# Performance work log

Hardware: AMD Instinct MI355X
Metric: run time of the kernel (lower is better)

The kernel has to match this reference:

```python
import jax, jax.numpy as jnp
import numpy as np

B, S, D, H = 4, 2048, 1024, 16
HS = D // H  # head size = 64


def setup_inputs() -> dict:
    key = jax.random.key(0)
    k1, k2, k3 = jax.random.split(key, 3)
    return {
        "input_data": jax.random.normal(k1, (B, S, D), dtype=jnp.float32),
        "w_qkv": jax.random.normal(k2, (D, 3 * D), dtype=jnp.float32) * (1.0 / np.sqrt(D)),
        "b_qkv": jnp.zeros((3 * D,), dtype=jnp.float32),
        "w_proj": jax.random.normal(k3, (D, D), dtype=jnp.float32) * (1.0 / np.sqrt(D)),
        "b_proj": jnp.zeros((D,), dtype=jnp.float32),
    }


def reference(input_data, w_qkv, b_qkv, w_proj, b_proj):
    b, s, d = input_data.shape
    qkv = input_data @ w_qkv + b_qkv  # [b, s, 3d]
    q, k, v = jnp.split(qkv, 3, axis=-1)
    # [b, h, s, hs]
    q = q.reshape(b, s, H, HS).transpose(0, 2, 1, 3)
    k = k.reshape(b, s, H, HS).transpose(0, 2, 1, 3)
    v = v.reshape(b, s, H, HS).transpose(0, 2, 1, 3)
    # NB: original module scales by 1/sqrt(num_heads), not 1/sqrt(head_size)
    scores = jnp.einsum('bhqd,bhkd->bhqk', q, k) / jnp.sqrt(jnp.float32(H))
    causal = jnp.tril(jnp.ones((s, s), dtype=bool))
    scores = jnp.where(causal[None, None], scores, -jnp.inf)
    weights = jax.nn.softmax(scores, axis=-1)  # dropout p=0.0 -> identity
    out = jnp.einsum('bhqk,bhkd->bhqd', weights, v)
    out = out.transpose(0, 2, 1, 3).reshape(b, s, d)
    return out @ w_proj + b_proj
```

## Files before the change

kernel.cpp:

```cpp
#include <hip/hip_runtime.h>


typedef unsigned short u16;
typedef short bf16x8 __attribute__((ext_vector_type(8)));
typedef unsigned short u16x8 __attribute__((ext_vector_type(8)));
typedef float f32x4 __attribute__((ext_vector_type(4)));
typedef float f32x16 __attribute__((ext_vector_type(16)));

#define S_LEN 2048
#define DMODEL 1024
#define NHEAD 16
#define MROWS 8192

#define SCALE_LOG2E 0.36067376022224085f
#define DEFER_THR 8.0f

__device__ __forceinline__ u16 f2bf(float f) {
  union { float f; unsigned u; } c; c.f = f;
  unsigned u = c.u;
  u += 0x7fffu + ((u >> 16) & 1u);
  return (u16)(u >> 16);
}

__device__ __forceinline__ float exp2_fast(float x) {
  float r; asm("v_exp_f32 %0, %1" : "=v"(r) : "v"(x)); return r;
}

__device__ __forceinline__ unsigned cvtpk_bf16(float a, float b) {
  unsigned r;
  asm("v_cvt_pk_bf16_f32 %0, %1, %2" : "=v"(r) : "v"(a), "v"(b));
  return r;
}

__device__ __forceinline__ void plswap(unsigned& a, unsigned& b) {
  asm("v_permlane32_swap_b32 %0, %1" : "+v"(a), "+v"(b));
}

__device__ __forceinline__ f32x4 mfma16(bf16x8 a, bf16x8 b, f32x4 c) {
  return __builtin_amdgcn_mfma_f32_16x16x32_bf16(a, b, c, 0, 0, 0);
}

__device__ __forceinline__ f32x16 mfma32(bf16x8 a, bf16x8 b, f32x16 c) {
  return __builtin_amdgcn_mfma_f32_32x32x16_bf16(a, b, c, 0, 0, 0);
}

__device__ __forceinline__ void gload_lds16(const void* g, void* l) {
  __builtin_amdgcn_global_load_lds((__attribute__((address_space(1))) void*)g,
                                   (__attribute__((address_space(3))) void*)l,
                                   16, 0, 0);
}

__global__ void k_f32_to_bf16(const float* __restrict__ in, u16* __restrict__ out, int n) {
  int i = (blockIdx.x * 256 + threadIdx.x) * 4;
  if (i < n) {
    float4 v = *reinterpret_cast<const float4*>(in + i);
    ushort4 o;
    o.x = f2bf(v.x); o.y = f2bf(v.y); o.z = f2bf(v.z); o.w = f2bf(v.w);
    *reinterpret_cast<ushort4*>(out + i) = o;
  }
}

__global__ void k_transpose_to_bf16(const float* __restrict__ in, u16* __restrict__ out,
                                    int K, int N) {
  __shared__ float t[32][33];
  int n0 = blockIdx.x * 32, k0 = blockIdx.y * 32;
  int tx = threadIdx.x & 31, ty = threadIdx.x >> 5;
#pragma unroll
  for (int i = 0; i < 32; i += 8)
    t[ty + i][tx] = in[(size_t)(k0 + ty + i) * N + n0 + tx];
  __syncthreads();
#pragma unroll
  for (int i = 0; i < 32; i += 8)
    out[(size_t)(n0 + ty + i) * K + k0 + tx] = f2bf(t[tx][ty + i]);
}

template <int MODE>
__global__ __launch_bounds__(512, 1) void k_gemm8(const u16* __restrict__ A,
                                                  const u16* __restrict__ Bt,
                                                  const float* __restrict__ bias,
                                                  u16* __restrict__ outb,
                                                  float* __restrict__ outf,
                                                  u16* __restrict__ vtout,
                                                  int N, int K) {
  __shared__ u16 As[2][2][256 * 32];
  __shared__ u16 Bs[2][2][128 * 32];

  const int tid = threadIdx.x;
  const int lane = tid & 63, wave = tid >> 6;
  const int wr = wave >> 1, wc = wave & 1;
  const int lr = lane & 15, lk = lane >> 4;
  const int m0 = blockIdx.x * 256, n0 = blockIdx.y * 128;
  const size_t Kb = (size_t)K * 2;

  const int csw = ((tid & 3) ^ ((tid >> 3) & 3)) * 16;
  const char* Asrc0 = (const char*)A + (size_t)(m0 + (tid >> 2)) * Kb + csw;
  const char* Asrc1 = Asrc0 + 128 * Kb;
  const char* Bsrc0 = (const char*)Bt + (size_t)(n0 + (tid >> 2)) * Kb + csw;

#define STAGE_KH(BUFX, KH, T)                                                  \
  {                                                                            \
    const size_t ko_ = (size_t)(T) * 128 + (KH) * 64;                          \
    gload_lds16(Asrc0 + ko_, &As[BUFX][KH][(size_t)tid * 8]);                  \
    gload_lds16(Asrc1 + ko_, &As[BUFX][KH][((size_t)tid + 512) * 8]);          \
    gload_lds16(Bsrc0 + ko_, &Bs[BUFX][KH][(size_t)tid * 8]);                  \
  }

  f32x4 zero4 = {0.f, 0.f, 0.f, 0.f};
  f32x4 acc[4][4];
#pragma unroll
  for (int m = 0; m < 4; ++m)
#pragma unroll
    for (int n = 0; n < 4; ++n) acc[m][n] = zero4;

  const int slotsw = (lr >> 1) & 3;

#define PHASE(BUFX, KH, T, DOSTAGE, VMZERO)                                    \
  {                                                                            \
    if (VMZERO) asm volatile("s_waitcnt vmcnt(0)" ::: "memory");               \
    else        asm volatile("s_waitcnt vmcnt(3)" ::: "memory");               \
    __builtin_amdgcn_s_barrier();                                              \
    __builtin_amdgcn_sched_barrier(0);                                         \
    bf16x8 af[4], bfr[4];                                                      \
    _Pragma("unroll") for (int m = 0; m < 4; ++m)                              \
        af[m] = *reinterpret_cast<const bf16x8*>(                              \
            &As[BUFX][KH][(wr * 64 + m * 16 + lr) * 32 + ((lk ^ slotsw) * 8)]);\
    _Pragma("unroll") for (int n = 0; n < 4; ++n)                              \
        bfr[n] = *reinterpret_cast<const bf16x8*>(                             \
            &Bs[BUFX][KH][(wc * 64 + n * 16 + lr) * 32 + ((lk ^ slotsw) * 8)]);\
    if (DOSTAGE) STAGE_KH((BUFX) ^ 1, KH, (T) + 1);                            \
    __builtin_amdgcn_sched_barrier(0);                                         \
    __builtin_amdgcn_s_setprio(1);                                             \
    _Pragma("unroll") for (int m = 0; m < 4; ++m)                              \
        _Pragma("unroll") for (int n = 0; n < 4; ++n)                          \
            acc[m][n] = mfma16(af[m], bfr[n], acc[m][n]);                      \
    __builtin_amdgcn_s_setprio(0);                                             \
  }

  const int nkt = K >> 6;
  STAGE_KH(0, 0, 0);
  STAGE_KH(0, 1, 0);

  for (int t = 0; t < nkt - 1; ++t) {
    const int buf = t & 1;
    PHASE(buf, 0, t, 1, 0);
    PHASE(buf, 1, t, 1, 0);
  }
  {
    const int buf = (nkt - 1) & 1;
    PHASE(buf, 0, nkt - 1, 0, 0);
    PHASE(buf, 1, nkt - 1, 0, 1);
  }
#undef PHASE
#undef STAGE_KH

#pragma unroll
  for (int n = 0; n < 4; ++n) {
    int col = n0 + wc * 64 + n * 16 + lr;
    float bv = bias[col];
#pragma unroll
    for (int m = 0; m < 4; ++m) {
      int rowb = m0 + wr * 64 + m * 16 + lk * 4;
      if (MODE == 1) {
#pragma unroll
        for (int r = 0; r < 4; ++r)
          outf[(size_t)(rowb + r) * N + col] = acc[m][n][r] + bv;
      } else {
        if (col < 2048) {
          const float qs = (col < 1024) ? SCALE_LOG2E : 1.0f;
#pragma unroll
          for (int r = 0; r < 4; ++r)
            outb[(size_t)(rowb + r) * 2048 + col] = f2bf((acc[m][n][r] + bv) * qs);
        } else {
          int hh = (col >> 6) & 15, dd = col & 63;
          int bb = rowb >> 11, ss = rowb & 2047;
          ushort4 o;
          o.x = f2bf(acc[m][n][0] + bv);
          o.y = f2bf(acc[m][n][1] + bv);
          o.z = f2bf(acc[m][n][2] + bv);
          o.w = f2bf(acc[m][n][3] + bv);
          *reinterpret_cast<ushort4*>(
              vtout + ((size_t)(bb * 16 + hh) * 64 + dd) * 2048 + ss) = o;
        }
      }
    }
  }
}

__global__ __launch_bounds__(512, 4) void k_attn7(const u16* __restrict__ qk,
                                                  const u16* __restrict__ vt,
                                                  u16* __restrict__ ao) {
  __shared__ u16 Ks[2][4096];
  __shared__ u16 Vs[2][4096];

  const int tid = threadIdx.x;
  const int lane = tid & 63, wave = tid >> 6;
  const int l31 = lane & 31, hi = lane >> 5;
  const int gid = blockIdx.x;
  const int bh = gid & 63;
  const int tq = gid >> 6;
  const int t = (tq < 4) ? tq : 11 - tq;
  const int b = bh >> 4, h = bh & 15;

  const int q0 = t * 256 + wave * 32;
  const int ktd = (q0 + 31) >> 6;
  const int KTMAX = 4 * t + 3;
  const int qrel = q0 + l31 - ktd * 64;

  bf16x8 qf[4];
  {
    const u16* qp = qk + ((size_t)b * S_LEN + q0 + l31) * 2048 + h * 64 + hi * 8;
#pragma unroll
    for (int ks = 0; ks < 4; ++ks)
      qf[ks] = *reinterpret_cast<const bf16x8*>(qp + ks * 16);
  }

  const int swzcol = 16 * ((lane & 7) ^ (lane >> 3));
  const char* kg = (const char*)qk + ((size_t)b * S_LEN) * 4096 + 2048 + h * 128 +
                   (size_t)(wave * 8 + (lane >> 3)) * 4096 + swzcol;
  const char* vg = (const char*)vt +
                   ((size_t)bh * 64 + wave * 8 + (lane >> 3)) * 4096 + swzcol;

#define STAGE(BUF, KT)                                                   \
  {                                                                      \
    gload_lds16(kg + (size_t)(KT) * 64 * 4096, &Ks[BUF][wave * 512]);    \
    gload_lds16(vg + (size_t)(KT) * 128, &Vs[BUF][wave * 512]);          \
  }

  f32x16 oT[2];
#pragma unroll
  for (int kb = 0; kb < 2; ++kb)
#pragma unroll
    for (int g = 0; g < 16; ++g) oT[kb][g] = 0.f;
  float m_i = -INFINITY;
  float l_i = 0.f;

  const int rsw = (l31 & 7) << 4;

  STAGE(0, 0);
  __syncthreads();
  int buf = 0;

  for (int kt = 0; kt <= KTMAX; ++kt) {
    if (kt < KTMAX) STAGE(buf ^ 1, kt + 1);

    if (kt <= ktd) {
      const char* Kb = (const char*)&Ks[buf][0];
      const char* Vb = (const char*)&Vs[buf][0];
      const bool masked = (kt == ktd);

      bf16x8 kf[2][4];
#pragma unroll
      for (int kb = 0; kb < 2; ++kb)
#pragma unroll
        for (int ks = 0; ks < 4; ++ks)
          kf[kb][ks] = *reinterpret_cast<const bf16x8*>(
              Kb + (kb * 32 + l31) * 128 + ((ks * 32 + hi * 16) ^ rsw));

      f32x16 sc[2];
#pragma unroll
      for (int kb = 0; kb < 2; ++kb) {
        sc[kb] = mfma32(kf[kb][0], qf[0], f32x16{});
#pragma unroll
        for (int ks = 1; ks < 4; ++ks) sc[kb] = mfma32(kf[kb][ks], qf[ks], sc[kb]);
      }

      bf16x8 vf[2][4];
#pragma unroll
      for (int kbd = 0; kbd < 2; ++kbd)
#pragma unroll
        for (int tt = 0; tt < 4; ++tt)
          vf[kbd][tt] = *reinterpret_cast<const bf16x8*>(
              Vb + (kbd * 32 + l31) * 128 + ((tt * 32 + hi * 16) ^ rsw));

      if (masked) {
#pragma unroll
        for (int kb = 0; kb < 2; ++kb)
#pragma unroll
          for (int g = 0; g < 16; ++g) {
            int key_ = kb * 32 + (g & 3) + ((g >> 2) << 3) + hi * 4;
            if (key_ > qrel) sc[kb][g] = -INFINITY;
          }
      }
      float mxa = fmaxf(sc[0][0], sc[0][4]), mxb = fmaxf(sc[0][1], sc[0][5]);
      float mxc = fmaxf(sc[0][2], sc[0][6]), mxd = fmaxf(sc[0][3], sc[0][7]);
#pragma unroll
      for (int g = 8; g < 16; g += 4) {
        mxa = fmaxf(mxa, sc[0][g]);     mxb = fmaxf(mxb, sc[0][g + 1]);
        mxc = fmaxf(mxc, sc[0][g + 2]); mxd = fmaxf(mxd, sc[0][g + 3]);
      }
#pragma unroll
      for (int g = 0; g < 16; g += 4) {
        mxa = fmaxf(mxa, sc[1][g]);     mxb = fmaxf(mxb, sc[1][g + 1]);
        mxc = fmaxf(mxc, sc[1][g + 2]); mxd = fmaxf(mxd, sc[1][g + 3]);
      }
      float mx = fmaxf(fmaxf(mxa, mxb), fmaxf(mxc, mxd));
      mx = fmaxf(mx, __shfl_xor(mx, 32, 64));
      if (__any(mx > m_i + DEFER_THR)) {
        float mn = fmaxf(m_i, mx);
        float c = exp2_fast(m_i - mn);
        m_i = mn;
        l_i *= c;
#pragma unroll
        for (int kb = 0; kb < 2; ++kb)
#pragma unroll
          for (int g = 0; g < 16; ++g) oT[kb][g] *= c;
      }
      float rsa = 0.f, rsb = 0.f, rsc = 0.f, rsd = 0.f;
      unsigned pk_[8][2];
#pragma unroll
      for (int kb = 0; kb < 2; ++kb)
#pragma unroll
        for (int s = 0; s < 4; ++s) {
          float p0 = exp2_fast(sc[kb][s * 4 + 0] - m_i);
          float p1 = exp2_fast(sc[kb][s * 4 + 1] - m_i);
          float p2 = exp2_fast(sc[kb][s * 4 + 2] - m_i);
          float p3 = exp2_fast(sc[kb][s * 4 + 3] - m_i);
          rsa += p0; rsb += p1; rsc += p2; rsd += p3;
          pk_[kb * 4 + s][0] = cvtpk_bf16(p0, p1);
          pk_[kb * 4 + s][1] = cvtpk_bf16(p2, p3);
        }
      float rs = (rsa + rsb) + (rsc + rsd);
      rs += __shfl_xor(rs, 32, 64);
      l_i += rs;

      bf16x8 pfr[4];
#pragma unroll
      for (int tt = 0; tt < 4; ++tt) {
        unsigned a0 = pk_[2 * tt][0], b0 = pk_[2 * tt + 1][0];
        unsigned a1 = pk_[2 * tt][1], b1 = pk_[2 * tt + 1][1];
        plswap(a0, b0);
        plswap(a1, b1);
        unsigned fr[4] = {a0, a1, b0, b1};
        pfr[tt] = *reinterpret_cast<const bf16x8*>(&fr[0]);
      }

#pragma unroll
      for (int tt = 0; tt < 4; ++tt) {
        oT[0] = mfma32(vf[0][tt], pfr[tt], oT[0]);
        oT[1] = mfma32(vf[1][tt], pfr[tt], oT[1]);
      }
    }

    __syncthreads();
    buf ^= 1;
  }
#undef STAGE

  {
    float inv = 1.f / l_i;
    u16* orow = ao + ((size_t)b * S_LEN + q0 + l31) * DMODEL + h * 64 + hi * 4;
#pragma unroll
    for (int kbd = 0; kbd < 2; ++kbd)
#pragma unroll
      for (int s = 0; s < 4; ++s) {
        unsigned w0 = cvtpk_bf16(oT[kbd][s * 4 + 0] * inv, oT[kbd][s * 4 + 1] * inv);
        unsigned w1 = cvtpk_bf16(oT[kbd][s * 4 + 2] * inv, oT[kbd][s * 4 + 3] * inv);
        *reinterpret_cast<unsigned*>(orow + kbd * 32 + s * 8) = w0;
        *reinterpret_cast<unsigned*>(orow + kbd * 32 + s * 8 + 2) = w1;
      }
  }
}

extern "C" void kernel_launch(void* const* d_in, const int* in_sizes, int n_in,
                              void* d_out, int out_size, void* d_ws, size_t ws_size,
                              hipStream_t stream) {
  const float* x = (const float*)d_in[0];
  const float* wqkv = (const float*)d_in[1];
  const float* bqkv = (const float*)d_in[2];
  const float* wproj = (const float*)d_in[3];
  const float* bproj = (const float*)d_in[4];
  float* out = (float*)d_out;

  char* ws = (char*)d_ws;
  u16* Xb     = (u16*)(ws);
  u16* Wqkvt  = (u16*)(ws + (size_t)16777216);
  u16* Wprojt = (u16*)(ws + (size_t)23068672);
  u16* QKb    = (u16*)(ws + (size_t)25165824);
  u16* Vt     = (u16*)(ws + (size_t)58720256);
  u16* AOb    = (u16*)(ws + (size_t)75497472);

  k_f32_to_bf16<<<MROWS * DMODEL / 4 / 256, 256, 0, stream>>>(x, Xb, MROWS * DMODEL);
  k_transpose_to_bf16<<<dim3(3072 / 32, 1024 / 32), 256, 0, stream>>>(wqkv, Wqkvt, 1024, 3072);
  k_transpose_to_bf16<<<dim3(1024 / 32, 1024 / 32), 256, 0, stream>>>(wproj, Wprojt, 1024, 1024);

  k_gemm8<2><<<dim3(MROWS / 256, 3072 / 128), 512, 0, stream>>>(
      Xb, Wqkvt, bqkv, QKb, nullptr, Vt, 3072, 1024);

  k_attn7<<<dim3(512), 512, 0, stream>>>(QKb, Vt, AOb);

  k_gemm8<1><<<dim3(MROWS / 256, DMODEL / 128), 512, 0, stream>>>(
      AOb, Wprojt, bproj, nullptr, out, nullptr, DMODEL, 1024);
}
```

Measured before the change: 186.4 us.

## Triple-buffer GEMM loads and process two key tiles per attention barrier

Result: slower. 201.1 us (+7.9%).

```diff
diff --git a/kernel.cpp b/kernel.cpp
--- a/kernel.cpp
+++ b/kernel.cpp
@@ -14,6 +14,9 @@
 
 #define SCALE_LOG2E 0.36067376022224085f
 #define DEFER_THR 8.0f
+
+#define WAITVM_(N) asm volatile("s_waitcnt vmcnt(" #N ")" ::: "memory")
+#define WAITVM(N) WAITVM_(N)
 
 __device__ __forceinline__ u16 f2bf(float f) {
   union { float f; unsigned u; } c; c.f = f;
@@ -82,8 +85,8 @@
                                                   float* __restrict__ outf,
                                                   u16* __restrict__ vtout,
                                                   int N, int K) {
-  __shared__ u16 As[2][2][256 * 32];
-  __shared__ u16 Bs[2][2][128 * 32];
+  __shared__ u16 As[3][2][256 * 32];
+  __shared__ u16 Bs[3][2][128 * 32];
 
   const int tid = threadIdx.x;
   const int lane = tid & 63, wave = tid >> 6;
@@ -114,10 +117,9 @@
 
   const int slotsw = (lr >> 1) & 3;
 
-#define PHASE(BUFX, KH, T, DOSTAGE, VMZERO)                                    \
+#define PHASE(BUFX, KH, VM, DOSTAGE, SBUF, ST)                                 \
   {                                                                            \
-    if (VMZERO) asm volatile("s_waitcnt vmcnt(0)" ::: "memory");               \
-    else        asm volatile("s_waitcnt vmcnt(3)" ::: "memory");               \
+    WAITVM(VM);                                                                \
     __builtin_amdgcn_s_barrier();                                              \
     __builtin_amdgcn_sched_barrier(0);                                         \
     bf16x8 af[4], bfr[4];                                                      \
@@ -127,7 +129,7 @@
     _Pragma("unroll") for (int n = 0; n < 4; ++n)                              \
         bfr[n] = *reinterpret_cast<const bf16x8*>(                             \
             &Bs[BUFX][KH][(wc * 64 + n * 16 + lr) * 32 + ((lk ^ slotsw) * 8)]);\
-    if (DOSTAGE) STAGE_KH((BUFX) ^ 1, KH, (T) + 1);                            \
+    if (DOSTAGE) STAGE_KH(SBUF, KH, ST);                                       \
     __builtin_amdgcn_sched_barrier(0);                                         \
     __builtin_amdgcn_s_setprio(1);                                             \
     _Pragma("unroll") for (int m = 0; m < 4; ++m)                              \
@@ -139,16 +141,24 @@
   const int nkt = K >> 6;
   STAGE_KH(0, 0, 0);
   STAGE_KH(0, 1, 0);
-
-  for (int t = 0; t < nkt - 1; ++t) {
-    const int buf = t & 1;
-    PHASE(buf, 0, t, 1, 0);
-    PHASE(buf, 1, t, 1, 0);
+  STAGE_KH(1, 0, 1);
+  STAGE_KH(1, 1, 1);
+
+  for (int t = 0; t < nkt - 2; ++t) {
+    const int bf3 = t % 3;
+    const int bn3 = (t + 2) % 3;
+    PHASE(bf3, 0, 6, 1, bn3, t + 2);
+    PHASE(bf3, 1, 9, 1, bn3, t + 2);
   }
   {
-    const int buf = (nkt - 1) & 1;
-    PHASE(buf, 0, nkt - 1, 0, 0);
-    PHASE(buf, 1, nkt - 1, 0, 1);
+    const int bf3 = (nkt - 2) % 3;
+    PHASE(bf3, 0, 6, 0, 0, 0);
+    PHASE(bf3, 1, 6, 0, 0, 0);
+  }
+  {
+    const int bf3 = (nkt - 1) % 3;
+    PHASE(bf3, 0, 0, 0, 0, 0);
+    PHASE(bf3, 1, 0, 0, 0, 0);
   }
 #undef PHASE
 #undef STAGE_KH
@@ -186,11 +196,11 @@
   }
 }
 
-__global__ __launch_bounds__(512, 4) void k_attn7(const u16* __restrict__ qk,
+__global__ __launch_bounds__(512, 4) void k_attn8(const u16* __restrict__ qk,
                                                   const u16* __restrict__ vt,
                                                   u16* __restrict__ ao) {
-  __shared__ u16 Ks[2][4096];
-  __shared__ u16 Vs[2][4096];
+  __shared__ u16 Ks[2][2][4096];
+  __shared__ u16 Vs[2][2][4096];
 
   const int tid = threadIdx.x;
   const int lane = tid & 63, wave = tid >> 6;
@@ -203,7 +213,7 @@
 
   const int q0 = t * 256 + wave * 32;
   const int ktd = (q0 + 31) >> 6;
-  const int KTMAX = 4 * t + 3;
+  const int ITMAX = 2 * t + 1;
   const int qrel = q0 + l31 - ktd * 64;
 
   bf16x8 qf[4];
@@ -220,10 +230,14 @@
   const char* vg = (const char*)vt +
                    ((size_t)bh * 64 + wave * 8 + (lane >> 3)) * 4096 + swzcol;
 
-#define STAGE(BUF, KT)                                                   \
+#define STAGE2(BUF, IT)                                                  \
   {                                                                      \
-    gload_lds16(kg + (size_t)(KT) * 64 * 4096, &Ks[BUF][wave * 512]);    \
-    gload_lds16(vg + (size_t)(KT) * 128, &Vs[BUF][wave * 512]);          \
+    const char* kg_ = kg + (size_t)(IT) * 128 * 4096;                    \
+    const char* vg_ = vg + (size_t)(IT) * 256;                           \
+    gload_lds16(kg_, &Ks[BUF][0][wave * 512]);                           \
+    gload_lds16(kg_ + (size_t)64 * 4096, &Ks[BUF][1][wave * 512]);       \
+    gload_lds16(vg_, &Vs[BUF][0][wave * 512]);                           \
+    gload_lds16(vg_ + 128, &Vs[BUF][1][wave * 512]);                     \
   }
 
   f32x16 oT[2];
@@ -236,115 +250,130 @@
 
   const int rsw = (l31 & 7) << 4;
 
-  STAGE(0, 0);
-  __syncthreads();
+  STAGE2(0, 0);
   int buf = 0;
 
-  for (int kt = 0; kt <= KTMAX; ++kt) {
-    if (kt < KTMAX) STAGE(buf ^ 1, kt + 1);
-
-    if (kt <= ktd) {
-      const char* Kb = (const char*)&Ks[buf][0];
-      const char* Vb = (const char*)&Vs[buf][0];
-      const bool masked = (kt == ktd);
-
-      bf16x8 kf[2][4];
-#pragma unroll
-      for (int kb = 0; kb < 2; ++kb)
-#pragma unroll
-        for (int ks = 0; ks < 4; ++ks)
-          kf[kb][ks] = *reinterpret_cast<const bf16x8*>(
-              Kb + (kb * 32 + l31) * 128 + ((ks * 32 + hi * 16) ^ rsw));
-
-      f32x16 sc[2];
-#pragma unroll
-      for (int kb = 0; kb < 2; ++kb) {
-        sc[kb] = mfma32(kf[kb][0], qf[0], f32x16{});
-#pragma unroll
-        for (int ks = 1; ks < 4; ++ks) sc[kb] = mfma32(kf[kb][ks], qf[ks], sc[kb]);
-      }
-
-      bf16x8 vf[2][4];
-#pragma unroll
-      for (int kbd = 0; kbd < 2; ++kbd)
-#pragma unroll
-        for (int tt = 0; tt < 4; ++tt)
-          vf[kbd][tt] = *reinterpret_cast<const bf16x8*>(
-              Vb + (kbd * 32 + l31) * 128 + ((tt * 32 + hi * 16) ^ rsw));
-
-      if (masked) {
+  for (int it = 0; it <= ITMAX; ++it) {
+    if (it < ITMAX) {
+      STAGE2(buf ^ 1, it + 1);
+      WAITVM(4);
+    } else {
+      WAITVM(0);
+    }
+    __builtin_amdgcn_s_barrier();
+    __builtin_amdgcn_sched_barrier(0);
+
+    for (int pass = 0; pass < 2; ++pass) {
+      const int sub = (wave & 1) ^ pass;
+      const int s64 = 2 * it + sub;
+      if (s64 <= ktd) {
+        const char* Kb = (const char*)&Ks[buf][sub][0];
+        const char* Vb = (const char*)&Vs[buf][sub][0];
+        const bool masked = (s64 == ktd);
+
+        bf16x8 kf[2][4];
 #pragma unroll
         for (int kb = 0; kb < 2; ++kb)
 #pragma unroll
-          for (int g = 0; g < 16; ++g) {
-            int key_ = kb * 32 + (g & 3) + ((g >> 2) << 3) + hi * 4;
-            if (key_ > qrel) sc[kb][g] = -INFINITY;
+          for (int ks = 0; ks < 4; ++ks)
+            kf[kb][ks] = *reinterpret_cast<const bf16x8*>(
+                Kb + (kb * 32 + l31) * 128 + ((ks * 32 + hi * 16) ^ rsw));
+
+        f32x16 sc[2];
+        __builtin_amdgcn_s_setprio(1);
+#pragma unroll
+        for (int kb = 0; kb < 2; ++kb) {
+          sc[kb] = mfma32(kf[kb][0], qf[0], f32x16{});
+#pragma unroll
+          for (int ks = 1; ks < 4; ++ks) sc[kb] = mfma32(kf[kb][ks], qf[ks], sc[kb]);
+        }
+        __builtin_amdgcn_s_setprio(0);
+
+        bf16x8 vf[2][4];
+#pragma unroll
+        for (int kbd = 0; kbd < 2; ++kbd)
+#pragma unroll
+          for (int tt = 0; tt < 4; ++tt)
+            vf[kbd][tt] = *reinterpret_cast<const bf16x8*>(
+                Vb + (kbd * 32 + l31) * 128 + ((tt * 32 + hi * 16) ^ rsw));
+
+        if (masked) {
+#pragma unroll
+          for (int kb = 0; kb < 2; ++kb)
+#pragma unroll
+            for (int g = 0; g < 16; ++g) {
+              int key_ = kb * 32 + (g & 3) + ((g >> 2) << 3) + hi * 4;
+              if (key_ > qrel) sc[kb][g] = -INFINITY;
+            }
+        }
+        float mxa = fmaxf(sc[0][0], sc[0][4]), mxb = fmaxf(sc[0][1], sc[0][5]);
+        float mxc = fmaxf(sc[0][2], sc[0][6]), mxd = fmaxf(sc[0][3], sc[0][7]);
+#pragma unroll
+        for (int g = 8; g < 16; g += 4) {
+          mxa = fmaxf(mxa, sc[0][g]);     mxb = fmaxf(mxb, sc[0][g + 1]);
+          mxc = fmaxf(mxc, sc[0][g + 2]); mxd = fmaxf(mxd, sc[0][g + 3]);
+        }
+#pragma unroll
+        for (int g = 0; g < 16; g += 4) {
+          mxa = fmaxf(mxa, sc[1][g]);     mxb = fmaxf(mxb, sc[1][g + 1]);
+          mxc = fmaxf(mxc, sc[1][g + 2]); mxd = fmaxf(mxd, sc[1][g + 3]);
+        }
+        float mx = fmaxf(fmaxf(mxa, mxb), fmaxf(mxc, mxd));
+        mx = fmaxf(mx, __shfl_xor(mx, 32, 64));
+        if (__any(mx > m_i + DEFER_THR)) {
+          float mn = fmaxf(m_i, mx);
+          float c = exp2_fast(m_i - mn);
+          m_i = mn;
+          l_i *= c;
+#pragma unroll
+          for (int kb = 0; kb < 2; ++kb)
+#pragma unroll
+            for (int g = 0; g < 16; ++g) oT[kb][g] *= c;
+        }
+        float rsa = 0.f, rsb = 0.f, rsc = 0.f, rsd = 0.f;
+        unsigned pk_[8][2];
+#pragma unroll
+        for (int kb = 0; kb < 2; ++kb)
+#pragma unroll
+          for (int s = 0; s < 4; ++s) {
+            float p0 = exp2_fast(sc[kb][s * 4 + 0] - m_i);
+            float p1 = exp2_fast(sc[kb][s * 4 + 1] - m_i);
+            float p2 = exp2_fast(sc[kb][s * 4 + 2] - m_i);
+            float p3 = exp2_fast(sc[kb][s * 4 + 3] - m_i);
+            rsa += p0; rsb += p1; rsc += p2; rsd += p3;
+            pk_[kb * 4 + s][0] = cvtpk_bf16(p0, p1);
+            pk_[kb * 4 + s][1] = cvtpk_bf16(p2, p3);
           }
-      }
-      float mxa = fmaxf(sc[0][0], sc[0][4]), mxb = fmaxf(sc[0][1], sc[0][5]);
-      float mxc = fmaxf(sc[0][2], sc[0][6]), mxd = fmaxf(sc[0][3], sc[0][7]);
-#pragma unroll
-      for (int g = 8; g < 16; g += 4) {
-        mxa = fmaxf(mxa, sc[0][g]);     mxb = fmaxf(mxb, sc[0][g + 1]);
-        mxc = fmaxf(mxc, sc[0][g + 2]); mxd = fmaxf(mxd, sc[0][g + 3]);
-      }
-#pragma unroll
-      for (int g = 0; g < 16; g += 4) {
-        mxa = fmaxf(mxa, sc[1][g]);     mxb = fmaxf(mxb, sc[1][g + 1]);
-        mxc = fmaxf(mxc, sc[1][g + 2]); mxd = fmaxf(mxd, sc[1][g + 3]);
-      }
-      float mx = fmaxf(fmaxf(mxa, mxb), fmaxf(mxc, mxd));
-      mx = fmaxf(mx, __shfl_xor(mx, 32, 64));
-      if (__any(mx > m_i + DEFER_THR)) {
-        float mn = fmaxf(m_i, mx);
-        float c = exp2_fast(m_i - mn);
-        m_i = mn;
-        l_i *= c;
-#pragma unroll
-        for (int kb = 0; kb < 2; ++kb)
-#pragma unroll
-          for (int g = 0; g < 16; ++g) oT[kb][g] *= c;
-      }
-      float rsa = 0.f, rsb = 0.f, rsc = 0.f, rsd = 0.f;
-      unsigned pk_[8][2];
-#pragma unroll
-      for (int kb = 0; kb < 2; ++kb)
-#pragma unroll
-        for (int s = 0; s < 4; ++s) {
-          float p0 = exp2_fast(sc[kb][s * 4 + 0] - m_i);
-          float p1 = exp2_fast(sc[kb][s * 4 + 1] - m_i);
-          float p2 = exp2_fast(sc[kb][s * 4 + 2] - m_i);
-          float p3 = exp2_fast(sc[kb][s * 4 + 3] - m_i);
-          rsa += p0; rsb += p1; rsc += p2; rsd += p3;
-          pk_[kb * 4 + s][0] = cvtpk_bf16(p0, p1);
-          pk_[kb * 4 + s][1] = cvtpk_bf16(p2, p3);
-        }
-      float rs = (rsa + rsb) + (rsc + rsd);
-      rs += __shfl_xor(rs, 32, 64);
-      l_i += rs;
-
-      bf16x8 pfr[4];
-#pragma unroll
-      for (int tt = 0; tt < 4; ++tt) {
-        unsigned a0 = pk_[2 * tt][0], b0 = pk_[2 * tt + 1][0];
-        unsigned a1 = pk_[2 * tt][1], b1 = pk_[2 * tt + 1][1];
-        plswap(a0, b0);
-        plswap(a1, b1);
-        unsigned fr[4] = {a0, a1, b0, b1};
-        pfr[tt] = *reinterpret_cast<const bf16x8*>(&fr[0]);
-      }
-
-#pragma unroll
-      for (int tt = 0; tt < 4; ++tt) {
-        oT[0] = mfma32(vf[0][tt], pfr[tt], oT[0]);
-        oT[1] = mfma32(vf[1][tt], pfr[tt], oT[1]);
+        float rs = (rsa + rsb) + (rsc + rsd);
+        rs += __shfl_xor(rs, 32, 64);
+        l_i += rs;
+
+        bf16x8 pfr[4];
+#pragma unroll
+        for (int tt = 0; tt < 4; ++tt) {
+          unsigned a0 = pk_[2 * tt][0], b0 = pk_[2 * tt + 1][0];
+          unsigned a1 = pk_[2 * tt][1], b1 = pk_[2 * tt + 1][1];
+          plswap(a0, b0);
+          plswap(a1, b1);
+          unsigned fr[4] = {a0, a1, b0, b1};
+          pfr[tt] = *reinterpret_cast<const bf16x8*>(&fr[0]);
+        }
+
+        __builtin_amdgcn_s_setprio(1);
+#pragma unroll
+        for (int tt = 0; tt < 4; ++tt) {
+          oT[0] = mfma32(vf[0][tt], pfr[tt], oT[0]);
+          oT[1] = mfma32(vf[1][tt], pfr[tt], oT[1]);
+        }
+        __builtin_amdgcn_s_setprio(0);
       }
     }
 
-    __syncthreads();
+    __builtin_amdgcn_sched_barrier(0);
+    __builtin_amdgcn_s_barrier();
     buf ^= 1;
   }
-#undef STAGE
+#undef STAGE2
 
   {
     float inv = 1.f / l_i;
@@ -386,7 +415,7 @@
   k_gemm8<2><<<dim3(MROWS / 256, 3072 / 128), 512, 0, stream>>>(
       Xb, Wqkvt, bqkv, QKb, nullptr, Vt, 3072, 1024);
 
-  k_attn7<<<dim3(512), 512, 0, stream>>>(QKb, Vt, AOb);
+  k_attn8<<<dim3(512), 512, 0, stream>>>(QKb, Vt, AOb);
 
   k_gemm8<1><<<dim3(MROWS / 256, DMODEL / 128), 512, 0, stream>>>(
       AOb, Wprojt, bproj, nullptr, out, nullptr, DMODEL, 1024);
```
